# Kernel optimization log

Measured on AMD Instinct MI355X. Metric: run time of the kernel, lower is better.

## Reference

```python
import jax, jax.numpy as jnp
import numpy as np

B, T1 = 256, 64            # batch, number of transition steps (T-1)
S, A = 128, 32             # state_size, action_size
BEL, HID, EMB = 1024, 1024, 1024
MIN_STD = 0.1


def _lin(key, out_dim, in_dim):
    k1, k2 = jax.random.split(key)
    s = 1.0 / np.sqrt(in_dim)
    W = jax.random.uniform(k1, (out_dim, in_dim), jnp.float32, -s, s)
    b = jax.random.uniform(k2, (out_dim,), jnp.float32, -s, s)
    return W, b


def setup_inputs() -> dict:
    key = jax.random.key(0)
    ks = jax.random.split(key, 16)
    W_sa, b_sa = _lin(ks[0], BEL, S + A)
    # GRUCell weights (torch layout: [3H, in]/[3H, H], gate order r,z,n)
    sg = 1.0 / np.sqrt(BEL)
    W_ih = jax.random.uniform(ks[1], (3 * BEL, BEL), jnp.float32, -sg, sg)
    W_hh = jax.random.uniform(ks[2], (3 * BEL, BEL), jnp.float32, -sg, sg)
    b_ih = jax.random.uniform(ks[3], (3 * BEL,), jnp.float32, -sg, sg)
    b_hh = jax.random.uniform(ks[4], (3 * BEL,), jnp.float32, -sg, sg)
    W_bp, b_bp = _lin(ks[5], HID, BEL)
    W_sp, b_sp = _lin(ks[6], 2 * S, HID)
    W_bq, b_bq = _lin(ks[7], HID, BEL + EMB)
    W_sq, b_sq = _lin(ks[8], 2 * S, HID)
    return {
        "prev_state": jax.random.normal(ks[9], (B, S), jnp.float32),
        "actions": jax.random.normal(ks[10], (T1, B, A), jnp.float32),
        "prev_belief": jax.random.normal(ks[11], (B, BEL), jnp.float32),
        "observations": jax.random.normal(ks[12], (T1, B, EMB), jnp.float32),
        "nonterminals": jnp.ones((T1, B, 1), jnp.float32),
        "prior_noise": jax.random.normal(ks[13], (T1, B, S), jnp.float32),
        "post_noise": jax.random.normal(ks[14], (T1, B, S), jnp.float32),
        "W_sa": W_sa, "b_sa": b_sa,
        "W_ih": W_ih, "W_hh": W_hh, "b_ih": b_ih, "b_hh": b_hh,
        "W_bp": W_bp, "b_bp": b_bp, "W_sp": W_sp, "b_sp": b_sp,
        "W_bq": W_bq, "b_bq": b_bq, "W_sq": W_sq, "b_sq": b_sq,
    }


def reference(prev_state, actions, prev_belief, observations, nonterminals,
              prior_noise, post_noise,
              W_sa, b_sa, W_ih, W_hh, b_ih, b_hh,
              W_bp, b_bp, W_sp, b_sp, W_bq, b_bq, W_sq, b_sq):
    # nonterminals[t-1] is applied for t>=1; t==0 uses no mask -> prepend ones
    nt_eff = jnp.concatenate([jnp.ones_like(nonterminals[:1]), nonterminals[:-1]], axis=0)

    def step(carry, inp):
        belief, state = carry
        a, obs, nt, pn, qn = inp
        s = state * nt
        x = jax.nn.relu(jnp.concatenate([s, a], axis=-1) @ W_sa.T + b_sa)
        h = belief * nt
        # torch GRUCell: gates r,z,n
        gi = x @ W_ih.T + b_ih
        gh = h @ W_hh.T + b_hh
        ir, iz, in_ = jnp.split(gi, 3, axis=-1)
        hr, hz, hn = jnp.split(gh, 3, axis=-1)
        r = jax.nn.sigmoid(ir + hr)
        z = jax.nn.sigmoid(iz + hz)
        n = jnp.tanh(in_ + r * hn)
        nb = (1.0 - z) * n + z * h  # new belief [B, BEL]
        # prior head
        hp = jax.nn.relu(nb @ W_bp.T + b_bp)
        pm, psd_raw = jnp.split(hp @ W_sp.T + b_sp, 2, axis=-1)
        psd = jax.nn.softplus(psd_raw) + MIN_STD
        ps = pm + psd * pn
        # posterior head
        hq = jax.nn.relu(jnp.concatenate([nb, obs], axis=-1) @ W_bq.T + b_bq)
        qm, qsd_raw = jnp.split(hq @ W_sq.T + b_sq, 2, axis=-1)
        qsd = jax.nn.softplus(qsd_raw) + MIN_STD
        qs = qm + qsd * qn
        return (nb, qs), (nb, ps, pm, psd, qs, qm, qsd)

    _, outs = jax.lax.scan(step, (prev_belief, prev_state),
                           (actions, observations, nt_eff, prior_noise, post_noise))
    beliefs, prior_states, prior_means, prior_stds, post_states, post_means, post_stds = outs
    return beliefs, prior_states, prior_means, prior_stds, post_states, post_means, post_stds
```

## Files before the change

kernel.cpp:

```cpp
#include <hip/hip_runtime.h>
#include <math.h>

constexpr int NB = 256, NT = 64, DS = 128, DA = 32, DB = 1024, DH = 1024, DE = 1024;
constexpr float MIN_STD = 0.1f;

constexpr size_t OUT_PS  = (size_t)NT * NB * DB;
constexpr size_t OUT_PM  = OUT_PS  + (size_t)NT * NB * DS;
constexpr size_t OUT_PSD = OUT_PM  + (size_t)NT * NB * DS;
constexpr size_t OUT_QS  = OUT_PSD + (size_t)NT * NB * DS;
constexpr size_t OUT_QM  = OUT_QS  + (size_t)NT * NB * DS;
constexpr size_t OUT_QSD = OUT_QM  + (size_t)NT * NB * DS;

typedef __attribute__((ext_vector_type(8))) short bf8_t;
typedef __attribute__((ext_vector_type(4))) float f4_t;
#define MFMA16(a, b, c) __builtin_amdgcn_mfma_f32_16x16x32_bf16((a), (b), (c), 0, 0, 0)
#define SWZ8(ch, row) ((ch & ~7) | ((ch & 7) ^ ((row) & 7)))

__device__ __forceinline__ short f2bf(float f) {
    union { float f; unsigned u; } v; v.f = f;
    unsigned r = v.u + 0x7FFF + ((v.u >> 16) & 1);
    return (short)(r >> 16);
}
__device__ __forceinline__ float bf2f(unsigned short h) {
    union { unsigned u; float f; } v; v.u = ((unsigned)h) << 16; return v.f;
}
__device__ __forceinline__ unsigned pack2(float a, float b) {
    return ((unsigned)(unsigned short)f2bf(a)) | (((unsigned)(unsigned short)f2bf(b)) << 16);
}
__device__ __forceinline__ float sigm(float x) { return 1.0f / (1.0f + __expf(-x)); }

__global__ __launch_bounds__(256) void k_cvt_all(
    const float* __restrict__ Wih, const float* __restrict__ Whh,
    const float* __restrict__ Wbp, const float* __restrict__ Wbq,
    const float* __restrict__ Wsp, const float* __restrict__ Wsq,
    const float* __restrict__ Wsa,
    short* dWbp, short* dWbq, short* dWsp, short* dWsq,
    short* dWsqsw, short* dWsasw, short* dWbqnb, short* dWihsw, short* dWhhsw)
{
    int i = blockIdx.x * 256 + threadIdx.x;
    if (i >= 1429504) return;
    if (i >= 512000 && i < 643072) {
        int il = i - 512000;
        int c = il >> 7, kc = il & 127;
        const float4* s4 = (const float4*)Wbq;
        float4 a = s4[(size_t)c * 512 + kc * 2], b = s4[(size_t)c * 512 + kc * 2 + 1];
        bf8_t v;
        v[0]=f2bf(a.x); v[1]=f2bf(a.y); v[2]=f2bf(a.z); v[3]=f2bf(a.w);
        v[4]=f2bf(b.x); v[5]=f2bf(b.y); v[6]=f2bf(b.z); v[7]=f2bf(b.w);
        ((bf8_t*)dWbqnb)[((size_t)((c >> 4) * 128 + kc)) * 16 + (c & 15)] = v;
        return;
    }
    const float* src; short* dst; int lo; bool sw = false; int swNCH = 0;
    if      (i <  131072) { src = Wbp; dst = dWbp; lo = 0; }
    else if (i <  393216) { src = Wbq; dst = dWbq; lo = 131072; }
    else if (i <  425984) { src = Wsp; dst = dWsp; lo = 393216; }
    else if (i <  458752) { src = Wsq; dst = dWsq; lo = 425984; }
    else if (i <  491520) { src = Wsq; dst = dWsqsw; lo = 458752; sw = true; swNCH = 128; }
    else if (i <  512000) { src = Wsa; dst = dWsasw; lo = 491520; sw = true; swNCH = 20; }
    else if (i < 1036288) { src = Wih; dst = dWihsw; lo = 643072;  sw = true; swNCH = 128; }
    else                  { src = Whh; dst = dWhhsw; lo = 1036288; sw = true; swNCH = 128; }
    int il = i - lo;
    const float4* s4 = (const float4*)src;
    float4 a = s4[il * 2], b = s4[il * 2 + 1];
    bf8_t v;
    v[0]=f2bf(a.x); v[1]=f2bf(a.y); v[2]=f2bf(a.z); v[3]=f2bf(a.w);
    v[4]=f2bf(b.x); v[5]=f2bf(b.y); v[6]=f2bf(b.z); v[7]=f2bf(b.w);
    if (!sw) ((bf8_t*)dst)[il] = v;
    else {
        int row = il / swNCH, ch = il % swNCH;
        ((bf8_t*)dst)[((row >> 4) * swNCH + ch) * 16 + (row & 15)] = v;
    }
}

__global__ __launch_bounds__(256) void kobs(
    const float* __restrict__ obsA, const short* __restrict__ Wbq_bf,
    const float* __restrict__ b_bq, short* __restrict__ dst)
{
    __shared__ __align__(16) char smem[16384];
    const int tx = threadIdx.x;
    const int wv = tx >> 6, lane = tx & 63;
    const int b0 = blockIdx.y * 64, j0 = blockIdx.x * 64;
    const int wm = wv & 1, wn = wv >> 1;
    const bf8_t* Wq8 = (const bf8_t*)Wbq_bf;
    bf8_t* sA = (bf8_t*)smem;
    bf8_t* sB = sA + 512;
    f4_t acc[2][2];
    acc[0][0] = (f4_t)0.0f; acc[0][1] = (f4_t)0.0f;
    acc[1][0] = (f4_t)0.0f; acc[1][1] = (f4_t)0.0f;

    for (int kt = 0; kt < DE; kt += 64) {
        #pragma unroll
        for (int i = 0; i < 2; ++i) {
            int c = tx + i * 256;
            int row = c >> 3, ch = c & 7;
            const float4* p4 = (const float4*)(obsA + (size_t)(b0 + row) * DE + kt + ch * 8);
            float4 f0 = p4[0], f1 = p4[1];
            bf8_t v;
            v[0]=f2bf(f0.x); v[1]=f2bf(f0.y); v[2]=f2bf(f0.z); v[3]=f2bf(f0.w);
            v[4]=f2bf(f1.x); v[5]=f2bf(f1.y); v[6]=f2bf(f1.z); v[7]=f2bf(f1.w);
            sA[row * 8 + (ch ^ (row & 7))] = v;
            sB[row * 8 + (ch ^ (row & 7))] = Wq8[(size_t)(j0 + row) * 256 + 128 + (kt >> 3) + ch];
        }
        __syncthreads();
        #pragma unroll
        for (int ks = 0; ks < 2; ++ks) {
            int ch = ks * 4 + (lane >> 4);
            bf8_t a[2], b[2];
            #pragma unroll
            for (int mi = 0; mi < 2; ++mi) {
                int row = wm * 32 + mi * 16 + (lane & 15);
                a[mi] = sA[row * 8 + (ch ^ (row & 7))];
            }
            #pragma unroll
            for (int ni = 0; ni < 2; ++ni) {
                int row = wn * 32 + ni * 16 + (lane & 15);
                b[ni] = sB[row * 8 + (ch ^ (row & 7))];
            }
            #pragma unroll
            for (int mi = 0; mi < 2; ++mi)
                #pragma unroll
                for (int ni = 0; ni < 2; ++ni)
                    acc[mi][ni] = MFMA16(a[mi], b[ni], acc[mi][ni]);
        }
        __syncthreads();
    }
    float* ebuf = (float*)smem;
    #pragma unroll
    for (int mi = 0; mi < 2; ++mi)
        #pragma unroll
        for (int ni = 0; ni < 2; ++ni)
            #pragma unroll
            for (int r = 0; r < 4; ++r) {
                int row = wm * 32 + mi * 16 + (lane >> 4) * 4 + r;
                int col = wn * 32 + ni * 16 + (lane & 15);
                ebuf[row * 64 + col] = acc[mi][ni][r] + b_bq[j0 + col];
            }
    __syncthreads();
    {
        int bl = tx >> 2, p = tx & 3;
        float* src = ebuf + bl * 64 + p * 16;
        short* d = dst + (size_t)(b0 + bl) * DB + j0 + p * 16;
        #pragma unroll
        for (int q = 0; q < 4; ++q) {
            uint2 u; u.x = pack2(src[q*4], src[q*4+1]); u.y = pack2(src[q*4+2], src[q*4+3]);
            *(uint2*)(d + q * 4) = u;
        }
    }
}

__global__ __launch_bounds__(1024) void kstep(
    int t,
    const float* __restrict__ prev_state, const float* __restrict__ actions_t,
    const float* __restrict__ nonterm, const float* __restrict__ post_noise,
    const short* __restrict__ part_in, const short* __restrict__ obs_pre_tm1,
    const short* __restrict__ Wsq_sw, const float* __restrict__ b_sq,
    const short* __restrict__ Wsa_sw, const float* __restrict__ b_sa,
    const short* __restrict__ Wih_sw, const short* __restrict__ Whh_sw,
    const float* __restrict__ b_ih, const float* __restrict__ b_hh,
    const short* __restrict__ Wbqnb_sw,
    const float* __restrict__ belp,
    float* __restrict__ bel_out, short* __restrict__ part_out,
    float* __restrict__ o_qm, float* __restrict__ o_qsd, float* __restrict__ o_qs)
{
    __shared__ __align__(16) char smem[124160];
    short* R1s = (short*)smem;
    bf8_t* R18 = (bf8_t*)smem;
    float* qex = (float*)smem;
    bf8_t* hf8 = (bf8_t*)(smem + 32768);
    bf8_t* sP  = (bf8_t*)(smem + 32768);
    short* saS = (short*)(smem + 65536);
    bf8_t* sa8 = (bf8_t*)(smem + 65536);
    float* exg = (float*)(smem + 70912);
    float* exn = (float*)(smem + 120064);

    const int tx = threadIdx.x, bid = blockIdx.x;
    const int wv = tx >> 6, lane = tx & 63;
    const int ar = lane & 15, kq = lane >> 4;
    const int bgrp = bid >> 4, low = bid & 15;
    const int jt = ((low & 7) << 1) | (low >> 3);
    const int b0 = bgrp * 16, j0 = jt * 64;
    const float* ntp = (t > 0) ? nonterm + (size_t)(t - 1) * NB : nullptr;

    if (t > 0) {
        #pragma unroll
        for (int i = 0; i < 2; ++i) {
            int c = tx + i * 1024;
            int row = c >> 7, ch = c & 127;
            const bf8_t o8 = ((const bf8_t*)obs_pre_tm1)[(size_t)(b0 + row) * 128 + ch];
            float s[8];
            #pragma unroll
            for (int e = 0; e < 8; ++e) s[e] = bf2f((unsigned short)o8[e]);
            #pragma unroll
            for (int p = 0; p < 16; ++p) {
                const bf8_t v = ((const bf8_t*)part_in)[((size_t)p * NB + b0 + row) * 128 + ch];
                #pragma unroll
                for (int e = 0; e < 8; ++e) s[e] += bf2f((unsigned short)v[e]);
            }
            bf8_t r;
            #pragma unroll
            for (int e = 0; e < 8; ++e) r[e] = f2bf(fmaxf(s[e], 0.0f));
            R18[row * 128 + SWZ8(ch, row)] = r;
        }
        __syncthreads();
        {
            f4_t qa[4];
            #pragma unroll
            for (int i = 0; i < 4; ++i) qa[i] = (f4_t)0.0f;
            for (int ks = 0; ks < 32; ks += 4) {
                #pragma unroll
                for (int u = 0; u < 4; ++u) {
                    int ch = (ks + u) * 4 + kq;
                    bf8_t a = R18[ar * 128 + SWZ8(ch, ar)];
                    bf8_t bfr = *(const bf8_t*)(Wsq_sw +
                        ((size_t)(wv * 128 + ch)) * 128 + ar * 8);
                    qa[u] = MFMA16(a, bfr, qa[u]);
                }
            }
            f4_t qs_ = (qa[0] + qa[1]) + (qa[2] + qa[3]);
            __syncthreads();
            #pragma unroll
            for (int r = 0; r < 4; ++r)
                qex[(kq * 4 + r) * 257 + wv * 16 + ar] = qs_[r];
        }
        __syncthreads();
        #pragma unroll
        for (int i = 0; i < 2; ++i) {
            int e = tx + i * 1024;
            int row = e >> 7, col = e & 127;
            int b = b0 + row;
            float m  = qex[row * 257 + col] + b_sq[col];
            float sr = qex[row * 257 + 128 + col] + b_sq[128 + col];
            float sd = log1pf(__expf(-fabsf(sr))) + fmaxf(sr, 0.0f) + MIN_STD;
            float n_ = post_noise[((size_t)(t - 1) * NB + b) * DS + col];
            float qs = fmaf(sd, n_, m);
            if (jt == 0) {
                size_t off = ((size_t)(t - 1) * NB + b) * DS + col;
                o_qm[off] = m; o_qsd[off] = sd; o_qs[off] = qs;
            }
            saS[row * 168 + col] = f2bf(qs * ntp[b]);
        }
    } else {
        #pragma unroll
        for (int i = 0; i < 2; ++i) {
            int e = tx + i * 1024;
            int row = e >> 7, col = e & 127;
            saS[row * 168 + col] = f2bf(prev_state[(size_t)(b0 + row) * DS + col]);
        }
    }
    if (tx < 512) {
        int row = tx >> 5, ac = tx & 31;
        saS[row * 168 + 128 + ac] = f2bf(actions_t[(size_t)(b0 + row) * DA + ac]);
    }
    __syncthreads();

    {
        f4_t xacc[4];
        #pragma unroll
        for (int i = 0; i < 4; ++i) xacc[i] = (f4_t)0.0f;
        #pragma unroll
        for (int ks = 0; ks < 5; ++ks) {
            int ch = ks * 4 + kq;
            bf8_t a = sa8[ar * 21 + ch];
            #pragma unroll
            for (int i = 0; i < 4; ++i) {
                int tile = wv * 4 + i;
                bf8_t bfr = *(const bf8_t*)(Wsa_sw +
                    ((size_t)(tile * 20 + ch)) * 128 + ar * 8);
                xacc[i] = MFMA16(a, bfr, xacc[i]);
            }
        }
        #pragma unroll
        for (int i = 0; i < 4; ++i) {
            int col = (wv * 4 + i) * 16 + ar;
            float bj = b_sa[col];
            int chunk = col >> 3, el = col & 7;
            #pragma unroll
            for (int r = 0; r < 4; ++r) {
                int row = kq * 4 + r;
                R1s[row * 1024 + SWZ8(chunk, row) * 8 + el] =
                    f2bf(fmaxf(xacc[i][r] + bj, 0.0f));
            }
        }
    }
    #pragma unroll
    for (int i = 0; i < 2; ++i) {
        int c = tx + i * 1024;
        int row = c >> 7, ch = c & 127;
        int b = b0 + row;
        const float4* p4 = (const float4*)(belp + (size_t)b * DB + ch * 8);
        float4 f0 = p4[0], f1 = p4[1];
        float ntv = ntp ? ntp[b] : 1.0f;
        bf8_t v;
        v[0]=f2bf(f0.x*ntv); v[1]=f2bf(f0.y*ntv); v[2]=f2bf(f0.z*ntv); v[3]=f2bf(f0.w*ntv);
        v[4]=f2bf(f1.x*ntv); v[5]=f2bf(f1.y*ntv); v[6]=f2bf(f1.z*ntv); v[7]=f2bf(f1.w*ntv);
        hf8[row * 128 + SWZ8(ch, row)] = v;
    }
    __syncthreads();

    {
        const int kh = wv >> 3, wg = (wv >> 2) & 1, wn = wv & 3;
        f4_t acc[3];
        acc[0] = (f4_t)0.0f; acc[1] = (f4_t)0.0f; acc[2] = (f4_t)0.0f;
        const bf8_t* Asrc = wg ? hf8 : R18;
        const short* Wsw = wg ? Whh_sw : Wih_sw;
        #pragma unroll 4
        for (int k16 = 0; k16 < 16; ++k16) {
            int chunk = kh * 64 + k16 * 4 + kq;
            bf8_t a = Asrc[ar * 128 + SWZ8(chunk, ar)];
            #pragma unroll
            for (int g = 0; g < 3; ++g) {
                bf8_t bfr = *(const bf8_t*)(Wsw +
                    (((size_t)(g * 64 + jt * 4 + wn) * 128 + chunk) * 16 + ar) * 8);
                acc[g] = MFMA16(a, bfr, acc[g]);
            }
        }
        #pragma unroll
        for (int g = 0; g < 3; ++g)
            #pragma unroll
            for (int r = 0; r < 4; ++r)
                exg[((wv * 3 + g) * 16 + (kq * 4 + r)) * 16 + ar] = acc[g][r];
    }
    __syncthreads();
    if (wv < 4) {
        const int wn2 = wv, cl = ar;
        const int j = j0 + wn2 * 16 + cl;
        const float bir = b_ih[j], biz = b_ih[DB + j], bin = b_ih[2 * DB + j];
        const float bhr = b_hh[j], bhz = b_hh[DB + j], bhn = b_hh[2 * DB + j];
        #pragma unroll
        for (int r = 0; r < 4; ++r) {
            const int row = kq * 4 + r;
            const int b = b0 + row;
            float gi[3], gh[3];
            #pragma unroll
            for (int g = 0; g < 3; ++g) {
                gi[g] = exg[(((0  + wn2) * 3 + g) * 16 + row) * 16 + cl]
                      + exg[(((8  + wn2) * 3 + g) * 16 + row) * 16 + cl];
                gh[g] = exg[(((4  + wn2) * 3 + g) * 16 + row) * 16 + cl]
                      + exg[(((12 + wn2) * 3 + g) * 16 + row) * 16 + cl];
            }
            const float ntv = ntp ? ntp[b] : 1.0f;
            const float h = belp[(size_t)b * DB + j] * ntv;
            const float rr = sigm(gi[0] + bir + gh[0] + bhr);
            const float zz = sigm(gi[1] + biz + gh[1] + bhz);
            const float nn = tanhf(gi[2] + bin + rr * (gh[2] + bhn));
            exn[row * 64 + wn2 * 16 + cl] = (1.0f - zz) * nn + zz * h;
        }
    }
    __syncthreads();
    {
        int row = tx >> 6, col = tx & 63;
        bel_out[(size_t)(b0 + row) * DB + j0 + col] = exn[row * 64 + col];
    }
    if (tx < 128) {
        int row = tx >> 3, ch = tx & 7;
        const float* s = exn + row * 64 + ch * 8;
        bf8_t v;
        v[0]=f2bf(s[0]); v[1]=f2bf(s[1]); v[2]=f2bf(s[2]); v[3]=f2bf(s[3]);
        v[4]=f2bf(s[4]); v[5]=f2bf(s[5]); v[6]=f2bf(s[6]); v[7]=f2bf(s[7]);
        sP[row * 8 + (ch ^ (row & 7))] = v;
    }
    __syncthreads();
    {
        f4_t pacc[4];
        #pragma unroll
        for (int i = 0; i < 4; ++i) pacc[i] = (f4_t)0.0f;
        #pragma unroll
        for (int ks = 0; ks < 2; ++ks) {
            int ch = ks * 4 + kq;
            bf8_t a = sP[ar * 8 + (ch ^ (ar & 7))];
            #pragma unroll
            for (int i = 0; i < 4; ++i) {
                int tile = wv * 4 + i;
                bf8_t bfr = *(const bf8_t*)(Wbqnb_sw +
                    (((size_t)tile * 128 + jt * 8 + ch) * 16 + ar) * 8);
                pacc[i] = MFMA16(a, bfr, pacc[i]);
            }
        }
        #pragma unroll
        for (int i = 0; i < 4; ++i) {
            int c = (wv * 4 + i) * 16 + ar;
            #pragma unroll
            for (int r = 0; r < 4; ++r)
                part_out[((size_t)jt * NB + b0 + kq * 4 + r) * DB + c] = f2bf(pacc[i][r]);
        }
    }
}

__global__ __launch_bounds__(256) void khq63(
    const short* __restrict__ partials, const short* __restrict__ obs_pre,
    short* __restrict__ hqb)
{
    const int row = blockIdx.x;
    const int c = threadIdx.x * 4;
    const ushort4 o = *(const ushort4*)(obs_pre + (size_t)row * DB + c);
    float s0 = bf2f(o.x), s1 = bf2f(o.y), s2 = bf2f(o.z), s3 = bf2f(o.w);
    for (int p = 0; p < 16; ++p) {
        const ushort4 v = *(const ushort4*)(partials + ((size_t)p * NB + row) * DB + c);
        s0 += bf2f(v.x); s1 += bf2f(v.y); s2 += bf2f(v.z); s3 += bf2f(v.w);
    }
    uint2 u;
    u.x = pack2(fmaxf(s0, 0.0f), fmaxf(s1, 0.0f));
    u.y = pack2(fmaxf(s2, 0.0f), fmaxf(s3, 0.0f));
    *(uint2*)(hqb + (size_t)row * DB + c) = u;
}

__global__ __launch_bounds__(256) void kout(
    const short* __restrict__ A_, const short* __restrict__ W_,
    const float* __restrict__ bias, const float* __restrict__ noise,
    float* __restrict__ om, float* __restrict__ osd, float* __restrict__ os)
{
    __shared__ __align__(16) char smem[12288];
    const int tx = threadIdx.x;
    const int wv = tx >> 6, lane = tx & 63;
    const int b0 = blockIdx.y * 64, i0 = blockIdx.x * 16;
    const int wm = wv & 1, wn = wv >> 1;
    const bf8_t* A8 = (const bf8_t*)A_;
    const bf8_t* W8 = (const bf8_t*)W_;
    bf8_t* sA = (bf8_t*)smem;
    bf8_t* sB = sA + 512;
    f4_t acc[2];
    acc[0] = (f4_t)0.0f; acc[1] = (f4_t)0.0f;

    for (int kt = 0; kt < DH; kt += 64) {
        #pragma unroll
        for (int i = 0; i < 2; ++i) {
            int c = tx + i * 256;
            int row = c >> 3, ch = c & 7;
            sA[row * 8 + (ch ^ (row & 7))] = A8[(size_t)(b0 + row) * 128 + (kt >> 3) + ch];
        }
        {
            int row = tx >> 3, ch = tx & 7;
            int wr = (row < 16) ? (i0 + row) : (128 + i0 + (row - 16));
            sB[row * 8 + (ch ^ (row & 7))] = W8[(size_t)wr * 128 + (kt >> 3) + ch];
        }
        __syncthreads();
        #pragma unroll
        for (int ks = 0; ks < 2; ++ks) {
            int ch = ks * 4 + (lane >> 4);
            bf8_t a[2], b;
            #pragma unroll
            for (int mi = 0; mi < 2; ++mi) {
                int row = wm * 32 + mi * 16 + (lane & 15);
                a[mi] = sA[row * 8 + (ch ^ (row & 7))];
            }
            {
                int row = wn * 16 + (lane & 15);
                b = sB[row * 8 + (ch ^ (row & 7))];
            }
            acc[0] = MFMA16(a[0], b, acc[0]);
            acc[1] = MFMA16(a[1], b, acc[1]);
        }
        __syncthreads();
    }
    float* ebuf = (float*)smem;
    #pragma unroll
    for (int mi = 0; mi < 2; ++mi)
        #pragma unroll
        for (int r = 0; r < 4; ++r) {
            int row = wm * 32 + mi * 16 + (lane >> 4) * 4 + r;
            int col = wn * 16 + (lane & 15);
            ebuf[row * 32 + col] = acc[mi][r];
        }
    __syncthreads();
    {
        int bl = tx >> 2, p = tx & 3;
        int b = b0 + bl;
        float4 vm, vs, vx;
        #pragma unroll
        for (int k = 0; k < 4; ++k) {
            int i = p * 4 + k;
            float m_ = ebuf[bl * 32 + i] + bias[i0 + i];
            float sraw = ebuf[bl * 32 + 16 + i] + bias[128 + i0 + i];
            float sd = log1pf(__expf(-fabsf(sraw))) + fmaxf(sraw, 0.0f) + MIN_STD;
            float n_ = noise[(size_t)b * DS + i0 + i];
            ((float*)&vm)[k] = m_;
            ((float*)&vs)[k] = sd;
            ((float*)&vx)[k] = fmaf(sd, n_, m_);
        }
        size_t off = (size_t)b * DS + i0 + p * 4;
        *(float4*)(om + off)  = vm;
        *(float4*)(osd + off) = vs;
        *(float4*)(os + off)  = vx;
    }
}

__global__ __launch_bounds__(256) void khp(
    const float* __restrict__ belA, const short* __restrict__ Wbp_bf,
    const float* __restrict__ b_bp, short* __restrict__ hp_bf)
{
    __shared__ __align__(16) char smem[16384];
    const int tx = threadIdx.x;
    const int wv = tx >> 6, lane = tx & 63;
    const int b0 = blockIdx.y * 64, j0 = blockIdx.x * 64;
    const int wm = wv & 1, wn = wv >> 1;
    const bf8_t* Wp8 = (const bf8_t*)Wbp_bf;
    bf8_t* sA = (bf8_t*)smem;
    bf8_t* sB = sA + 512;
    f4_t acc[2][2];
    acc[0][0] = (f4_t)0.0f; acc[0][1] = (f4_t)0.0f;
    acc[1][0] = (f4_t)0.0f; acc[1][1] = (f4_t)0.0f;

    for (int kt = 0; kt < DB; kt += 64) {
        #pragma unroll
        for (int i = 0; i < 2; ++i) {
            int c = tx + i * 256;
            int row = c >> 3, ch = c & 7;
            const float4* p4 = (const float4*)(belA + (size_t)(b0 + row) * DB + kt + ch * 8);
            float4 f0 = p4[0], f1 = p4[1];
            bf8_t v;
            v[0]=f2bf(f0.x); v[1]=f2bf(f0.y); v[2]=f2bf(f0.z); v[3]=f2bf(f0.w);
            v[4]=f2bf(f1.x); v[5]=f2bf(f1.y); v[6]=f2bf(f1.z); v[7]=f2bf(f1.w);
            sA[row * 8 + (ch ^ (row & 7))] = v;
            sB[row * 8 + (ch ^ (row & 7))] = Wp8[(size_t)(j0 + row) * 128 + (kt >> 3) + ch];
        }
        __syncthreads();
        #pragma unroll
        for (int ks = 0; ks < 2; ++ks) {
            int ch = ks * 4 + (lane >> 4);
            bf8_t a[2], b[2];
            #pragma unroll
            for (int mi = 0; mi < 2; ++mi) {
                int row = wm * 32 + mi * 16 + (lane & 15);
                a[mi] = sA[row * 8 + (ch ^ (row & 7))];
            }
            #pragma unroll
            for (int ni = 0; ni < 2; ++ni) {
                int row = wn * 32 + ni * 16 + (lane & 15);
                b[ni] = sB[row * 8 + (ch ^ (row & 7))];
            }
            #pragma unroll
            for (int mi = 0; mi < 2; ++mi)
                #pragma unroll
                for (int ni = 0; ni < 2; ++ni)
                    acc[mi][ni] = MFMA16(a[mi], b[ni], acc[mi][ni]);
        }
        __syncthreads();
    }
    float* ebuf = (float*)smem;
    #pragma unroll
    for (int mi = 0; mi < 2; ++mi)
        #pragma unroll
        for (int ni = 0; ni < 2; ++ni)
            #pragma unroll
            for (int r = 0; r < 4; ++r) {
                int row = wm * 32 + mi * 16 + (lane >> 4) * 4 + r;
                int col = wn * 32 + ni * 16 + (lane & 15);
                ebuf[row * 64 + col] = fmaxf(acc[mi][ni][r] + b_bp[j0 + col], 0.0f);
            }
    __syncthreads();
    {
        int bl = tx >> 2, p = tx & 3;
        float* src = ebuf + bl * 64 + p * 16;
        short* dst = hp_bf + (size_t)(b0 + bl) * DH + j0 + p * 16;
        #pragma unroll
        for (int q = 0; q < 4; ++q) {
            uint2 u; u.x = pack2(src[q*4], src[q*4+1]); u.y = pack2(src[q*4+2], src[q*4+3]);
            *(uint2*)(dst + q * 4) = u;
        }
    }
}

extern "C" void kernel_launch(void* const* d_in, const int* in_sizes, int n_in,
                              void* d_out, int out_size, void* d_ws, size_t ws_size,
                              hipStream_t stream)
{
    const float* prev_state   = (const float*)d_in[0];
    const float* actions      = (const float*)d_in[1];
    const float* prev_belief  = (const float*)d_in[2];
    const float* observations = (const float*)d_in[3];
    const float* nonterm      = (const float*)d_in[4];
    const float* prior_noise  = (const float*)d_in[5];
    const float* post_noise   = (const float*)d_in[6];
    const float* W_sa = (const float*)d_in[7];
    const float* b_sa = (const float*)d_in[8];
    const float* W_ih = (const float*)d_in[9];
    const float* W_hh = (const float*)d_in[10];
    const float* b_ih = (const float*)d_in[11];
    const float* b_hh = (const float*)d_in[12];
    const float* W_bp = (const float*)d_in[13];
    const float* b_bp = (const float*)d_in[14];
    const float* W_sp = (const float*)d_in[15];
    const float* b_sp = (const float*)d_in[16];
    const float* W_bq = (const float*)d_in[17];
    const float* b_bq = (const float*)d_in[18];
    const float* W_sq = (const float*)d_in[19];
    const float* b_sq = (const float*)d_in[20];

    float* out     = (float*)d_out;
    float* beliefs = out;
    float* o_ps  = out + OUT_PS;
    float* o_pm  = out + OUT_PM;
    float* o_psd = out + OUT_PSD;
    float* o_qs  = out + OUT_QS;
    float* o_qm  = out + OUT_QM;
    float* o_qsd = out + OUT_QSD;

    short* w = (short*)d_ws;
    short* Wbp_bf   = w;
    short* Wbq_bf   = Wbp_bf   + (size_t)1048576;
    short* Wsp_bf   = Wbq_bf   + (size_t)2097152;
    short* Wsq_bf   = Wsp_bf   + (size_t)262144;
    short* Wsq_sw   = Wsq_bf   + (size_t)262144;
    short* Wsa_sw   = Wsq_sw   + (size_t)262144;
    short* Wbqnb_sw = Wsa_sw   + (size_t)163840;
    short* Wih_sw   = Wbqnb_sw + (size_t)1048576;
    short* Whh_sw   = Wih_sw   + (size_t)3145728;
    short* obs_ch   = Whh_sw   + (size_t)3145728;
    short* partials = obs_ch   + (size_t)4194304;
    short* hqb      = partials + (size_t)8388608;
    short* hp_bf    = hqb      + (size_t)262144;
    const size_t PART = (size_t)16 * NB * DB;

    k_cvt_all<<<5584, 256, 0, stream>>>(
        W_ih, W_hh, W_bp, W_bq, W_sp, W_sq, W_sa,
        Wbp_bf, Wbq_bf, Wsp_bf, Wsq_bf, Wsq_sw, Wsa_sw, Wbqnb_sw, Wih_sw, Whh_sw);

    for (int t = 0; t < NT; ++t) {
        const float* belp = (t == 0) ? prev_belief : beliefs + (size_t)(t - 1) * NB * DB;
        kstep<<<256, 1024, 0, stream>>>(
            t, prev_state, actions + (size_t)t * NB * DA,
            nonterm, post_noise,
            partials + ((t & 1) ^ 1) * PART,
            obs_ch + (size_t)((t + 15) & 15) * NB * DB,
            Wsq_sw, b_sq, Wsa_sw, b_sa,
            Wih_sw, Whh_sw, b_ih, b_hh, Wbqnb_sw,
            belp, beliefs + (size_t)t * NB * DB,
            partials + (t & 1) * PART,
            o_qm, o_qsd, o_qs);
        if ((t & 15) == 0)
            kobs<<<dim3(16, 64), 256, 0, stream>>>(
                observations + (size_t)t * NB * DE, Wbq_bf, b_bq, obs_ch);
    }

    khq63<<<256, 256, 0, stream>>>(
        partials + ((NT - 1) & 1) * PART, obs_ch + (size_t)15 * NB * DB, hqb);
    kout<<<dim3(8, 4), 256, 0, stream>>>(
        hqb, Wsq_bf, b_sq, post_noise + (size_t)(NT - 1) * NB * DS,
        o_qm + (size_t)(NT - 1) * NB * DS, o_qsd + (size_t)(NT - 1) * NB * DS,
        o_qs + (size_t)(NT - 1) * NB * DS);

    for (int c = 0; c < 4; ++c) {
        const size_t r0 = (size_t)c * 4096;
        khp<<<dim3(16, 64), 256, 0, stream>>>(
            beliefs + r0 * DB, Wbp_bf, b_bp, hp_bf);
        kout<<<dim3(8, 64), 256, 0, stream>>>(
            hp_bf, Wsp_bf, b_sp, prior_noise + r0 * DS,
            o_pm + r0 * DS, o_psd + r0 * DS, o_ps + r0 * DS);
    }
}
```

Baseline: 2.723 ms.

## Precompute all observation projections upfront, parallelize GRU epilogue across all threads

After: 2.611 ms. 1.04x faster.

```diff
diff --git a/kernel.cpp b/kernel.cpp
--- a/kernel.cpp
+++ b/kernel.cpp
@@ -162,16 +162,16 @@
     float* __restrict__ bel_out, short* __restrict__ part_out,
     float* __restrict__ o_qm, float* __restrict__ o_qsd, float* __restrict__ o_qs)
 {
-    __shared__ __align__(16) char smem[124160];
+    __shared__ __align__(16) char smem[120064];
     short* R1s = (short*)smem;
     bf8_t* R18 = (bf8_t*)smem;
     float* qex = (float*)smem;
     bf8_t* hf8 = (bf8_t*)(smem + 32768);
     bf8_t* sP  = (bf8_t*)(smem + 32768);
+    short* sPs = (short*)(smem + 32768);
     short* saS = (short*)(smem + 65536);
     bf8_t* sa8 = (bf8_t*)(smem + 65536);
     float* exg = (float*)(smem + 70912);
-    float* exn = (float*)(smem + 120064);
 
     const int tx = threadIdx.x, bid = blockIdx.x;
     const int wv = tx >> 6, lane = tx & 63;
@@ -321,43 +321,28 @@
                 exg[((wv * 3 + g) * 16 + (kq * 4 + r)) * 16 + ar] = acc[g][r];
     }
     __syncthreads();
-    if (wv < 4) {
-        const int wn2 = wv, cl = ar;
-        const int j = j0 + wn2 * 16 + cl;
-        const float bir = b_ih[j], biz = b_ih[DB + j], bin = b_ih[2 * DB + j];
-        const float bhr = b_hh[j], bhz = b_hh[DB + j], bhn = b_hh[2 * DB + j];
-        #pragma unroll
-        for (int r = 0; r < 4; ++r) {
-            const int row = kq * 4 + r;
-            const int b = b0 + row;
-            float gi[3], gh[3];
-            #pragma unroll
-            for (int g = 0; g < 3; ++g) {
-                gi[g] = exg[(((0  + wn2) * 3 + g) * 16 + row) * 16 + cl]
-                      + exg[(((8  + wn2) * 3 + g) * 16 + row) * 16 + cl];
-                gh[g] = exg[(((4  + wn2) * 3 + g) * 16 + row) * 16 + cl]
-                      + exg[(((12 + wn2) * 3 + g) * 16 + row) * 16 + cl];
-            }
-            const float ntv = ntp ? ntp[b] : 1.0f;
-            const float h = belp[(size_t)b * DB + j] * ntv;
-            const float rr = sigm(gi[0] + bir + gh[0] + bhr);
-            const float zz = sigm(gi[1] + biz + gh[1] + bhz);
-            const float nn = tanhf(gi[2] + bin + rr * (gh[2] + bhn));
-            exn[row * 64 + wn2 * 16 + cl] = (1.0f - zz) * nn + zz * h;
-        }
-    }
-    __syncthreads();
     {
-        int row = tx >> 6, col = tx & 63;
-        bel_out[(size_t)(b0 + row) * DB + j0 + col] = exn[row * 64 + col];
-    }
-    if (tx < 128) {
-        int row = tx >> 3, ch = tx & 7;
-        const float* s = exn + row * 64 + ch * 8;
-        bf8_t v;
-        v[0]=f2bf(s[0]); v[1]=f2bf(s[1]); v[2]=f2bf(s[2]); v[3]=f2bf(s[3]);
-        v[4]=f2bf(s[4]); v[5]=f2bf(s[5]); v[6]=f2bf(s[6]); v[7]=f2bf(s[7]);
-        sP[row * 8 + (ch ^ (row & 7))] = v;
+        const int row = tx >> 6;
+        const int col = tx & 63;
+        const int wn2 = col >> 4, cl = col & 15;
+        const int j = j0 + col;
+        float gi[3], gh[3];
+        #pragma unroll
+        for (int g = 0; g < 3; ++g) {
+            gi[g] = exg[(((0  + wn2) * 3 + g) * 16 + row) * 16 + cl]
+                  + exg[(((8  + wn2) * 3 + g) * 16 + row) * 16 + cl];
+            gh[g] = exg[(((4  + wn2) * 3 + g) * 16 + row) * 16 + cl]
+                  + exg[(((12 + wn2) * 3 + g) * 16 + row) * 16 + cl];
+        }
+        const int b = b0 + row;
+        const float ntv = ntp ? ntp[b] : 1.0f;
+        const float h = belp[(size_t)b * DB + j] * ntv;
+        const float rr = sigm(gi[0] + b_ih[j] + gh[0] + b_hh[j]);
+        const float zz = sigm(gi[1] + b_ih[DB + j] + gh[1] + b_hh[DB + j]);
+        const float nn = tanhf(gi[2] + b_ih[2 * DB + j] + rr * (gh[2] + b_hh[2 * DB + j]));
+        const float nbv = (1.0f - zz) * nn + zz * h;
+        bel_out[(size_t)b * DB + j] = nbv;
+        sPs[row * 64 + ((((col >> 3) ^ (row & 7)) << 3) | (col & 7))] = f2bf(nbv);
     }
     __syncthreads();
     {
@@ -605,15 +590,17 @@
     short* Wbqnb_sw = Wsa_sw   + (size_t)163840;
     short* Wih_sw   = Wbqnb_sw + (size_t)1048576;
     short* Whh_sw   = Wih_sw   + (size_t)3145728;
-    short* obs_ch   = Whh_sw   + (size_t)3145728;
-    short* partials = obs_ch   + (size_t)4194304;
+    short* obs_all  = Whh_sw   + (size_t)3145728;
+    short* partials = obs_all  + (size_t)16777216;
     short* hqb      = partials + (size_t)8388608;
-    short* hp_bf    = hqb      + (size_t)262144;
+    short* hp_bf    = partials;
     const size_t PART = (size_t)16 * NB * DB;
 
     k_cvt_all<<<5584, 256, 0, stream>>>(
         W_ih, W_hh, W_bp, W_bq, W_sp, W_sq, W_sa,
         Wbp_bf, Wbq_bf, Wsp_bf, Wsq_bf, Wsq_sw, Wsa_sw, Wbqnb_sw, Wih_sw, Whh_sw);
+
+    kobs<<<dim3(16, 256), 256, 0, stream>>>(observations, Wbq_bf, b_bq, obs_all);
 
     for (int t = 0; t < NT; ++t) {
         const float* belp = (t == 0) ? prev_belief : beliefs + (size_t)(t - 1) * NB * DB;
@@ -621,29 +608,26 @@
             t, prev_state, actions + (size_t)t * NB * DA,
             nonterm, post_noise,
             partials + ((t & 1) ^ 1) * PART,
-            obs_ch + (size_t)((t + 15) & 15) * NB * DB,
+            obs_all + (size_t)(t > 0 ? t - 1 : 0) * NB * DB,
             Wsq_sw, b_sq, Wsa_sw, b_sa,
             Wih_sw, Whh_sw, b_ih, b_hh, Wbqnb_sw,
             belp, beliefs + (size_t)t * NB * DB,
             partials + (t & 1) * PART,
             o_qm, o_qsd, o_qs);
-        if ((t & 15) == 0)
-            kobs<<<dim3(16, 64), 256, 0, stream>>>(
-                observations + (size_t)t * NB * DE, Wbq_bf, b_bq, obs_ch);
     }
 
     khq63<<<256, 256, 0, stream>>>(
-        partials + ((NT - 1) & 1) * PART, obs_ch + (size_t)15 * NB * DB, hqb);
+        partials + ((NT - 1) & 1) * PART, obs_all + (size_t)(NT - 1) * NB * DB, hqb);
     kout<<<dim3(8, 4), 256, 0, stream>>>(
         hqb, Wsq_bf, b_sq, post_noise + (size_t)(NT - 1) * NB * DS,
         o_qm + (size_t)(NT - 1) * NB * DS, o_qsd + (size_t)(NT - 1) * NB * DS,
         o_qs + (size_t)(NT - 1) * NB * DS);
 
-    for (int c = 0; c < 4; ++c) {
-        const size_t r0 = (size_t)c * 4096;
-        khp<<<dim3(16, 64), 256, 0, stream>>>(
+    for (int c = 0; c < 2; ++c) {
+        const size_t r0 = (size_t)c * 8192;
+        khp<<<dim3(16, 128), 256, 0, stream>>>(
             beliefs + r0 * DB, Wbp_bf, b_bp, hp_bf);
-        kout<<<dim3(8, 64), 256, 0, stream>>>(
+        kout<<<dim3(8, 128), 256, 0, stream>>>(
             hp_bf, Wsp_bf, b_sp, prior_noise + r0 * DS,
             o_pm + r0 * DS, o_psd + r0 * DS, o_ps + r0 * DS);
     }
```
